# Optimization experiments

Measured on AMD Instinct MI355X. Metric: run time of the kernel, lower is better.

The kernel has to match this reference:

```python
import jax, jax.numpy as jnp
import numpy as np

N_SKILLS = 1000
N_PROBLEMS = 20000
EMB = 256
TIME_LOG = 5.0
B, S = 32, 2048


def setup_inputs() -> dict:
    key = jax.random.key(0)
    ks = jax.random.split(key, 10)
    skills = jax.random.randint(ks[0], (B, S), 0, N_SKILLS, dtype=jnp.int64) if jax.config.jax_enable_x64 else jax.random.randint(ks[0], (B, S), 0, N_SKILLS, dtype=jnp.int32)
    problems = jax.random.randint(ks[1], (B, S), 0, N_PROBLEMS, dtype=skills.dtype)
    times = jnp.sort(jax.random.randint(ks[2], (B, S), 0, 10_000_000, dtype=skills.dtype), axis=-1)
    labels = jax.random.randint(ks[3], (B, S), 0, 2, dtype=skills.dtype)
    std = 0.01
    alpha_inter_W = std * jax.random.normal(ks[4], (2 * N_SKILLS, EMB), dtype=jnp.float32)
    alpha_skill_W = std * jax.random.normal(ks[5], (N_SKILLS, EMB), dtype=jnp.float32)
    beta_inter_W = std * jax.random.normal(ks[6], (2 * N_SKILLS, EMB), dtype=jnp.float32)
    beta_skill_W = std * jax.random.normal(ks[7], (N_SKILLS, EMB), dtype=jnp.float32)
    problem_base_W = std * jax.random.normal(ks[8], (N_PROBLEMS, 1), dtype=jnp.float32)
    skill_base_W = std * jax.random.normal(ks[9], (N_SKILLS, 1), dtype=jnp.float32)
    return {
        "skills": skills, "problems": problems, "times": times, "labels": labels,
        "alpha_inter_W": alpha_inter_W, "alpha_skill_W": alpha_skill_W,
        "beta_inter_W": beta_inter_W, "beta_skill_W": beta_skill_W,
        "problem_base_W": problem_base_W, "skill_base_W": skill_base_W,
    }


def reference(skills, problems, times, labels,
              alpha_inter_W, alpha_skill_W, beta_inter_W, beta_skill_W,
              problem_base_W, skill_base_W):
    n_skills = alpha_skill_W.shape[0]
    inters = skills + labels * n_skills  # [B,S]

    alpha_src = alpha_inter_W[inters]      # [B,S,E]
    alpha_tgt = alpha_skill_W[skills]      # [B,S,E]
    alphas = jnp.einsum("bse,bte->bst", alpha_src, alpha_tgt)  # [B,S,S]

    beta_src = beta_inter_W[inters]
    beta_tgt = beta_skill_W[skills]
    betas = jnp.einsum("bse,bte->bst", beta_src, beta_tgt)
    betas = jnp.clip(betas + 1.0, 0.0, 10.0)

    t = times.astype(jnp.float32) / 1000.0
    delta_t = jnp.abs(t[:, :, None] - t[:, None, :])
    delta_t = jnp.log(delta_t + 1e-10) / jnp.log(jnp.float32(TIME_LOG))

    cross = alphas * jnp.exp(-betas * delta_t)  # [B,S,S]

    seq_len = skills.shape[1]
    # original keeps strict upper triangle (source i strictly before target j)
    keep = jnp.triu(jnp.ones((seq_len, seq_len), dtype=cross.dtype), k=1)
    sum_t = jnp.sum(cross * keep[None], axis=-2)  # sum over source dim -> [B,S]

    problem_bias = problem_base_W[problems][..., 0]  # [B,S]
    skill_bias = skill_base_W[skills][..., 0]        # [B,S]
    h = problem_bias + skill_bias + sum_t
    return jax.nn.sigmoid(h)
```

## Files before the change

### kernel.cpp

```cpp
#include <hip/hip_runtime.h>
#include <hip/hip_bf16.h>
#include <stdint.h>

#define NSK   1000
#define EMB   256
#define BB    32
#define SS    2048
#define TI    128
#define TJ    64
#define NUNITB 272
#define BK    32
#define NCHUNK (EMB / BK)
#define LDSB  12288
#define SCALE_INV (1.0f / 4096.0f)

typedef float f32x16 __attribute__((ext_vector_type(16)));
typedef float f32x4  __attribute__((ext_vector_type(4)));
typedef long  longx2 __attribute__((ext_vector_type(2)));

#define OFF_AI8 0
#define OFF_BI8 (2 * NSK * EMB)
#define OFF_AS8 (4 * NSK * EMB)
#define OFF_BS8 (5 * NSK * EMB)
#define TOT8    (6 * NSK * EMB)

__global__ void cvt_tables(const float* __restrict__ ai, const float* __restrict__ bi,
                           const float* __restrict__ as_, const float* __restrict__ bs,
                           int* __restrict__ ws8, float* __restrict__ acc) {
    int g = blockIdx.x * 256 + threadIdx.x;
    if (g < BB * SS) acc[g] = 0.0f;
    if (g * 4 >= TOT8) return;
    int e = g * 4;
    const float* src; int off;
    if (e < OFF_AS8) { if (e < OFF_BI8) { src = ai;  off = e; }
                       else             { src = bi;  off = e - OFF_BI8; } }
    else             { if (e < OFF_BS8) { src = as_; off = e - OFF_AS8; }
                       else             { src = bs;  off = e - OFF_BS8; } }
    const float4 v = *(const float4*)(src + off);
    int lo = __builtin_amdgcn_cvt_pk_fp8_f32(v.x * 64.0f, v.y * 64.0f, 0, false);
    int wd = __builtin_amdgcn_cvt_pk_fp8_f32(v.z * 64.0f, v.w * 64.0f, lo, true);
    ws8[g] = wd;
}

__device__ __attribute__((noinline)) float dot256(const float* __restrict__ a,
                                                  const float* __restrict__ b) {
    float s = 0.0f;
#pragma unroll 8
    for (int k = 0; k < EMB; ++k) s += a[k] * b[k];
    return s;
}

__global__ __launch_bounds__(256, 4) void hawkes_unit(
    const int* __restrict__ skills, const int* __restrict__ times,
    const int* __restrict__ labels, const unsigned char* __restrict__ tab,
    const float* __restrict__ aiW_f, const float* __restrict__ asW_f,
    const float* __restrict__ biW_f, const float* __restrict__ bsW_f,
    float* __restrict__ acc)
{
    __shared__ __align__(16) char  sbuf[2 * LDSB];
    __shared__ __align__(16) float t_i[TI];
    __shared__ __align__(16) float t_j[TJ];
    __shared__ int   idx_i[TI];
    __shared__ int   idx_j[TJ];
    __shared__ float colsum[TJ];

    const int u  = blockIdx.x;
    const int b  = u / NUNITB;
    const int p  = u - b * NUNITB;
    int m = (int)sqrtf((float)p);
    while ((m + 1) * (m + 2) <= p) ++m;
    while (m * (m + 1) > p) --m;
    int jt, it;
    if (p >= (m + 1) * (m + 1)) { jt = 2 * m + 1; it = p - (m + 1) * (m + 1); }
    else                        { jt = 2 * m;     it = p - m * (m + 1); }
    const int j0 = jt * TJ, i0 = it * TI;
    const bool partial = (i0 + TI - 1 >= j0);

    const int tid = threadIdx.x;
    const int l   = tid & 63;
    const int w   = tid >> 6;
    const int wi  = w >> 1, wj = w & 1;
    const int lane31 = l & 31;
    const int khalf  = l >> 5;

    if (tid < TJ) {
        int j = j0 + tid;
        idx_j[tid] = skills[b * SS + j];
        t_j[tid]   = (float)times[b * SS + j] / 1000.0f;
        colsum[tid] = 0.0f;
    } else if (tid < TJ + TI) {
        int q = tid - TJ;
        int ii = i0 + q;
        idx_i[q] = skills[b * SS + ii] + labels[b * SS + ii] * NSK;
        t_i[q]   = (float)times[b * SS + ii] / 1000.0f;
    }
    __syncthreads();

    const float tjv = t_j[wj * 32 + lane31];
    const int   jl  = wj * 32 + lane31;

    const unsigned char* rowptr[3];
    int wo[3];
#pragma unroll
    for (int s = 0; s < 3; ++s) {
        int mm = w * 3 + s;
        int tabbase, ldsbase, row;
        if (mm < 8) {
            int mb = mm & 3;
            tabbase = (mm < 4) ? OFF_AI8 : OFF_BI8;
            ldsbase = ((mm < 4) ? 0 : 4096) + mb * 1024;
            row = idx_i[mb * 32 + (l >> 1)];
        } else {
            int mb = mm & 1;
            tabbase = (mm < 10) ? OFF_AS8 : OFF_BS8;
            ldsbase = ((mm < 10) ? 8192 : 10240) + mb * 1024;
            row = idx_j[mb * 32 + (l >> 1)];
        }
        rowptr[s] = tab + tabbase + (size_t)row * EMB + (l & 1) * 16;
        wo[s] = ldsbase + (l & 1) * 512 + (l >> 1) * 8;
    }

#define LOADC(dst, c)                                                  \
    do { _Pragma("unroll")                                             \
        for (int s = 0; s < 3; ++s)                                    \
            dst[s] = *(const longx2*)(rowptr[s] + (c) * BK);           \
    } while (0)
#define WRITEC(src, buf)                                               \
    do { char* db = sbuf + (buf) * LDSB;                               \
        _Pragma("unroll")                                              \
        for (int s = 0; s < 3; ++s) {                                  \
            *(long*)(db + wo[s])       = src[s].x;                     \
            *(long*)(db + wo[s] + 256) = src[s].y;                     \
        }                                                              \
    } while (0)

    f32x16 accA[2], accB[2];
#pragma unroll
    for (int mi = 0; mi < 2; ++mi) { accA[mi] = 0.0f; accB[mi] = 0.0f; }

    longx2 sreg[3];
    LOADC(sreg, 0);
    WRITEC(sreg, 0);

    for (int c = 0; c < NCHUNK; ++c) {
        if (c + 1 < NCHUNK) LOADC(sreg, c + 1);
        __syncthreads();

        const char* sb = sbuf + (c & 1) * LDSB;
#pragma unroll
        for (int ks = 0; ks < 2; ++ks) {
            long fa[2], fb[2], ga, gb;
#pragma unroll
            for (int mi = 0; mi < 2; ++mi) {
                int mb2 = (wi * 2 + mi) * 1024 + ks * 512 + l * 8;
                fa[mi] = *(const long*)(sb + 0    + mb2);
                fb[mi] = *(const long*)(sb + 4096 + mb2);
            }
            {
                int nb2 = wj * 1024 + ks * 512 + l * 8;
                ga = *(const long*)(sb + 8192  + nb2);
                gb = *(const long*)(sb + 10240 + nb2);
            }
#pragma unroll
            for (int mi = 0; mi < 2; ++mi) {
                accA[mi] = __builtin_amdgcn_mfma_f32_32x32x16_fp8_fp8(
                    fa[mi], ga, accA[mi], 0, 0, 0);
                accB[mi] = __builtin_amdgcn_mfma_f32_32x32x16_fp8_fp8(
                    fb[mi], gb, accB[mi], 0, 0, 0);
            }
        }

        if (c + 1 < NCHUNK) WRITEC(sreg, (c + 1) & 1);
    }

    float csum = 0.0f;
#pragma unroll
    for (int mi = 0; mi < 2; ++mi) {
        const int rbase = (wi * 2 + mi) * 32 + 4 * khalf;
        f32x4 tiv[4];
#pragma unroll
        for (int q = 0; q < 4; ++q) tiv[q] = *(const f32x4*)(t_i + rbase + 8 * q);
#pragma unroll
        for (int r = 0; r < 16; ++r) {
            const int q = r >> 2, e = r & 3;
            const int il = rbase + 8 * q + e;
            if (partial && i0 + il >= j0 + jl) continue;
            float d = fabsf(tiv[q][e] - tjv);
            float alpha, braw;
            if (d == 0.0f) {
                alpha = dot256(aiW_f + (size_t)idx_i[il] * EMB,
                               asW_f + (size_t)idx_j[jl] * EMB) * 4096.0f;
                braw  = dot256(biW_f + (size_t)idx_i[il] * EMB,
                               bsW_f + (size_t)idx_j[jl] * EMB) * 4096.0f;
            } else {
                alpha = accA[mi][r];
                braw  = accB[mi][r];
            }
            float dl   = __builtin_amdgcn_logf(d + 1e-10f) * 0.6213349345596119f;
            float beta = braw * SCALE_INV + 1.0f;
            csum += alpha * __builtin_amdgcn_exp2f(-beta * dl);
        }
    }
    csum *= SCALE_INV;

    __syncthreads();
    csum += __shfl_xor(csum, 32);
    if (l < 32)
        atomicAdd(&colsum[wj * 32 + lane31], csum);
    __syncthreads();
    if (tid < TJ)
        atomicAdd(&acc[b * SS + j0 + tid], colsum[tid]);
}

__global__ void hawkes_final(const int* __restrict__ skills, const int* __restrict__ problems,
                             const float* __restrict__ pbW, const float* __restrict__ sbW,
                             float* __restrict__ out) {
    int i = blockIdx.x * 256 + threadIdx.x;
    if (i >= BB * SS) return;
    float h = pbW[problems[i]] + sbW[skills[i]] + out[i];
    out[i] = 1.0f / (1.0f + __builtin_amdgcn_exp2f(-h * 1.4426950408889634f));
}

extern "C" void kernel_launch(void* const* d_in, const int* in_sizes, int n_in,
                              void* d_out, int out_size, void* d_ws, size_t ws_size,
                              hipStream_t stream) {
    const int*   skills   = (const int*)d_in[0];
    const int*   problems = (const int*)d_in[1];
    const int*   times    = (const int*)d_in[2];
    const int*   labels   = (const int*)d_in[3];
    const float* aiW      = (const float*)d_in[4];
    const float* asW      = (const float*)d_in[5];
    const float* biW      = (const float*)d_in[6];
    const float* bsW      = (const float*)d_in[7];
    const float* pbW      = (const float*)d_in[8];
    const float* sbW      = (const float*)d_in[9];
    float* out = (float*)d_out;
    unsigned char* tab = (unsigned char*)d_ws;

    cvt_tables<<<(TOT8 / 4 + 255) / 256, 256, 0, stream>>>(aiW, biW, asW, bsW,
                                                           (int*)tab, out);
    hawkes_unit<<<BB * NUNITB, 256, 0, stream>>>(skills, times, labels, tab,
                                                 aiW, asW, biW, bsW, out);
    hawkes_final<<<(BB * SS + 255) / 256, 256, 0, stream>>>(skills, problems, pbW, sbW, out);
}
```

Measured before the change: 181.7 us.

## Stage full-K alpha then beta operands in LDS instead of chunked double-buffering

Replaces the 8-chunk double-buffered K loop with two phases. Each phase loads the full 256-wide rows for the alpha tables, then for the beta tables, into a 48KB LDS buffer, with wider per-thread global loads (four 16-byte loads per slot). The beta loads are issued into registers while the alpha MFMAs run. This removes the per-chunk barriers and interleaving overhead. In exchange it uses more LDS and registers, and launch bounds drop from 4 to 3 waves, which lowers occupancy.

```diff
diff --git a/kernel.cpp b/kernel.cpp
--- a/kernel.cpp
+++ b/kernel.cpp
@@ -9,10 +9,10 @@
 #define TI    128
 #define TJ    64
 #define NUNITB 272
-#define BK    32
-#define NCHUNK (EMB / BK)
-#define LDSB  12288
 #define SCALE_INV (1.0f / 4096.0f)
+
+#define LDS_S   32768
+#define LDS_TOT 49152
 
 typedef float f32x16 __attribute__((ext_vector_type(16)));
 typedef float f32x4  __attribute__((ext_vector_type(4)));
@@ -50,14 +50,14 @@
     return s;
 }
 
-__global__ __launch_bounds__(256, 4) void hawkes_unit(
+__global__ __launch_bounds__(256, 3) void hawkes_unit(
     const int* __restrict__ skills, const int* __restrict__ times,
     const int* __restrict__ labels, const unsigned char* __restrict__ tab,
     const float* __restrict__ aiW_f, const float* __restrict__ asW_f,
     const float* __restrict__ biW_f, const float* __restrict__ bsW_f,
     float* __restrict__ acc)
 {
-    __shared__ __align__(16) char  sbuf[2 * LDSB];
+    __shared__ __align__(16) char  sbuf[LDS_TOT];
     __shared__ __align__(16) float t_i[TI];
     __shared__ __align__(16) float t_j[TJ];
     __shared__ int   idx_i[TI];
@@ -99,78 +99,90 @@
     const float tjv = t_j[wj * 32 + lane31];
     const int   jl  = wj * 32 + lane31;
 
-    const unsigned char* rowptr[3];
-    int wo[3];
+    const unsigned char* gA[3];
+    int bdel[3], usd[3], L0[3];
+    const int rg = l >> 2, sub = l & 3;
 #pragma unroll
     for (int s = 0; s < 3; ++s) {
-        int mm = w * 3 + s;
-        int tabbase, ldsbase, row;
-        if (mm < 8) {
-            int mb = mm & 3;
-            tabbase = (mm < 4) ? OFF_AI8 : OFF_BI8;
-            ldsbase = ((mm < 4) ? 0 : 4096) + mb * 1024;
-            row = idx_i[mb * 32 + (l >> 1)];
+        int slot = w * 48 + s * 16 + rg;
+        if (slot < TI) {
+            int row = idx_i[slot];
+            gA[s]   = tab + OFF_AI8 + (size_t)row * EMB + sub * 16;
+            bdel[s] = OFF_BI8 - OFF_AI8;
+            usd[s]  = 1024;
+            L0[s]   = sub * 2 * 1024 + slot * 8;
         } else {
-            int mb = mm & 1;
-            tabbase = (mm < 10) ? OFF_AS8 : OFF_BS8;
-            ldsbase = ((mm < 10) ? 8192 : 10240) + mb * 1024;
-            row = idx_j[mb * 32 + (l >> 1)];
-        }
-        rowptr[s] = tab + tabbase + (size_t)row * EMB + (l & 1) * 16;
-        wo[s] = ldsbase + (l & 1) * 512 + (l >> 1) * 8;
-    }
-
-#define LOADC(dst, c)                                                  \
+            int row = idx_j[slot - TI];
+            gA[s]   = tab + OFF_AS8 + (size_t)row * EMB + sub * 16;
+            bdel[s] = OFF_BS8 - OFF_AS8;
+            usd[s]  = 512;
+            L0[s]   = LDS_S + sub * 2 * 512 + (slot - TI) * 8;
+        }
+    }
+
+#define STAGE_WRITE(vv)                                                \
     do { _Pragma("unroll")                                             \
-        for (int s = 0; s < 3; ++s)                                    \
-            dst[s] = *(const longx2*)(rowptr[s] + (c) * BK);           \
-    } while (0)
-#define WRITEC(src, buf)                                               \
-    do { char* db = sbuf + (buf) * LDSB;                               \
-        _Pragma("unroll")                                              \
         for (int s = 0; s < 3; ++s) {                                  \
-            *(long*)(db + wo[s])       = src[s].x;                     \
-            *(long*)(db + wo[s] + 256) = src[s].y;                     \
+            _Pragma("unroll")                                          \
+            for (int i = 0; i < 4; ++i) {                              \
+                char* pp = sbuf + L0[s] + i * 8 * usd[s];              \
+                *(long*)(pp)          = vv[s][i].x;                    \
+                *(long*)(pp + usd[s]) = vv[s][i].y;                    \
+            }                                                          \
         }                                                              \
     } while (0)
 
+    longx2 vA[3][4];
+#pragma unroll
+    for (int s = 0; s < 3; ++s)
+#pragma unroll
+        for (int i = 0; i < 4; ++i)
+            vA[s][i] = *(const longx2*)(gA[s] + i * 64);
+    STAGE_WRITE(vA);
+    __syncthreads();
+
+    longx2 vB[3][4];
+#pragma unroll
+    for (int s = 0; s < 3; ++s)
+#pragma unroll
+        for (int i = 0; i < 4; ++i)
+            vB[s][i] = *(const longx2*)(gA[s] + bdel[s] + i * 64);
+
     f32x16 accA[2], accB[2];
 #pragma unroll
     for (int mi = 0; mi < 2; ++mi) { accA[mi] = 0.0f; accB[mi] = 0.0f; }
 
-    longx2 sreg[3];
-    LOADC(sreg, 0);
-    WRITEC(sreg, 0);
-
-    for (int c = 0; c < NCHUNK; ++c) {
-        if (c + 1 < NCHUNK) LOADC(sreg, c + 1);
-        __syncthreads();
-
-        const char* sb = sbuf + (c & 1) * LDSB;
-#pragma unroll
-        for (int ks = 0; ks < 2; ++ks) {
-            long fa[2], fb[2], ga, gb;
-#pragma unroll
-            for (int mi = 0; mi < 2; ++mi) {
-                int mb2 = (wi * 2 + mi) * 1024 + ks * 512 + l * 8;
-                fa[mi] = *(const long*)(sb + 0    + mb2);
-                fb[mi] = *(const long*)(sb + 4096 + mb2);
-            }
-            {
-                int nb2 = wj * 1024 + ks * 512 + l * 8;
-                ga = *(const long*)(sb + 8192  + nb2);
-                gb = *(const long*)(sb + 10240 + nb2);
-            }
-#pragma unroll
-            for (int mi = 0; mi < 2; ++mi) {
-                accA[mi] = __builtin_amdgcn_mfma_f32_32x32x16_fp8_fp8(
-                    fa[mi], ga, accA[mi], 0, 0, 0);
-                accB[mi] = __builtin_amdgcn_mfma_f32_32x32x16_fp8_fp8(
-                    fb[mi], gb, accB[mi], 0, 0, 0);
-            }
-        }
-
-        if (c + 1 < NCHUNK) WRITEC(sreg, (c + 1) & 1);
+    const int arow8 = (wi * 64 + lane31) * 8;
+    const int jrow8 = (wj * 32 + lane31) * 8;
+
+#pragma unroll
+    for (int ks = 0; ks < 16; ++ks) {
+        const int ib = ks * 2048 + khalf * 1024 + arow8;
+        const int sbo = LDS_S + ks * 1024 + khalf * 512 + jrow8;
+        long ga = *(const long*)(sbuf + sbo);
+#pragma unroll
+        for (int mi = 0; mi < 2; ++mi) {
+            long fa = *(const long*)(sbuf + ib + mi * 256);
+            accA[mi] = __builtin_amdgcn_mfma_f32_32x32x16_fp8_fp8(
+                fa, ga, accA[mi], 0, 0, 0);
+        }
+    }
+    __syncthreads();
+
+    STAGE_WRITE(vB);
+    __syncthreads();
+
+#pragma unroll
+    for (int ks = 0; ks < 16; ++ks) {
+        const int ib = ks * 2048 + khalf * 1024 + arow8;
+        const int sbo = LDS_S + ks * 1024 + khalf * 512 + jrow8;
+        long gb = *(const long*)(sbuf + sbo);
+#pragma unroll
+        for (int mi = 0; mi < 2; ++mi) {
+            long fb = *(const long*)(sbuf + ib + mi * 256);
+            accB[mi] = __builtin_amdgcn_mfma_f32_32x32x16_fp8_fp8(
+                fb, gb, accB[mi], 0, 0, 0);
+        }
     }
 
     float csum = 0.0f;
```

Result: slower. 193.9 us (+6.7%).
